# Kernel tuning notes

Measured on AMD Instinct MI355X. Metric: run time of the kernel, lower is better.

## Reference

```python
import jax, jax.numpy as jnp
import numpy as np

B, T, H, W = 8, 16, 512, 512
N, C = 300000, 128
STRIDE_B, STRIDE_T, STRIDE_H = T * H * W, H * W, W
SENTINEL = B * STRIDE_B  # out-of-range linear index used as unique fill_value


def setup_inputs() -> dict:
    key = jax.random.key(0)
    ks = jax.random.split(key, 8)
    # Random valid voxel coordinates via decomposed random linear index
    lin = jax.random.randint(ks[0], (N,), 0, SENTINEL, dtype=jnp.int32)
    b = lin // STRIDE_B
    r = lin % STRIDE_B
    t = r // STRIDE_T
    r = r % STRIDE_T
    y = r // STRIDE_H
    x = r % STRIDE_H
    indices = jnp.stack([b, t, y, x], axis=1).astype(jnp.int32)  # [N,4]
    s = 0.02
    return {
        "feats": jax.random.normal(ks[1], (N, C), jnp.float32),
        "indices": indices,
        "W1": jax.random.normal(ks[2], (C, C), jnp.float32) * s,
        "ln1_g": jnp.ones((C,), jnp.float32),
        "ln1_b": jnp.zeros((C,), jnp.float32),
        "W2": jax.random.normal(ks[3], (C, C), jnp.float32) * s,
        "ln2_g": jnp.ones((C,), jnp.float32),
        "ln2_b": jnp.zeros((C,), jnp.float32),
        "se_w1": jax.random.normal(ks[4], (C, C // 4), jnp.float32) * s,
        "se_b1": jnp.zeros((C // 4,), jnp.float32),
        "se_w2": jax.random.normal(ks[5], (C // 4, C), jnp.float32) * s,
        "se_b2": jnp.zeros((C,), jnp.float32),
    }


def _layernorm(x, g, b, eps=1e-5):
    mu = jnp.mean(x, axis=-1, keepdims=True)
    var = jnp.mean((x - mu) ** 2, axis=-1, keepdims=True)
    return (x - mu) * jax.lax.rsqrt(var + eps) * g + b


def reference(feats, indices, W1, ln1_g, ln1_b, W2, ln2_g, ln2_b,
              se_w1, se_b1, se_w2, se_b2):
    # conv1 (SubMConv3d k=1 == per-voxel linear) -> LayerNorm -> ReLU
    out = jax.nn.relu(_layernorm(feats @ W1, ln1_g, ln1_b))
    # conv2 -> LayerNorm
    out = _layernorm(out @ W2, ln2_g, ln2_b)
    # SE: global mean over all voxels -> fc -> relu -> fc -> sigmoid -> scale
    squeezed = jnp.mean(out, axis=0)                       # [C]
    scale = jax.nn.sigmoid(jax.nn.relu(squeezed @ se_w1 + se_b1) @ se_w2 + se_b2)
    out = out * scale
    # sparse_add(out, identity): linear hash, unique, scatter_add
    idx = indices.astype(jnp.int32)
    lin = (idx[:, 0] * STRIDE_B + idx[:, 1] * STRIDE_T
           + idx[:, 2] * STRIDE_H + idx[:, 3])             # [N]
    all_lin = jnp.concatenate([lin, lin])                  # [2N]
    all_feats = jnp.concatenate([out, feats])              # [2N, C]
    M = all_lin.shape[0]
    uniq, inv = jnp.unique(all_lin, size=M, fill_value=SENTINEL,
                           return_inverse=True)
    inv = inv.ravel()
    merged = jax.ops.segment_sum(all_feats, inv, num_segments=M)  # [2N, C]
    # decompose unique linear indices back to (b, t, y, x)
    cb = uniq // STRIDE_B
    r = uniq % STRIDE_B
    ct = r // STRIDE_T
    r = r % STRIDE_T
    ch = r // STRIDE_H
    cw = r % STRIDE_H
    comb_idx = jnp.stack([cb, ct, ch, cw], axis=1).astype(jnp.int32)
    # drop zero-feature / padded voxels (fixed-shape mask instead of compaction)
    valid = (jnp.abs(merged).sum(axis=1) > 1e-8) & (uniq < SENTINEL)
    merged = jnp.where(valid[:, None], merged, 0.0)
    merged = jax.nn.relu(merged)                           # lif2
    return merged, comb_idx, valid
```

## Files before the change

### kernel.cpp

```cpp
#include <hip/hip_runtime.h>
#include <cstdint>
#include <cstddef>

#define NVOX 300000
#define SB 4194304
#define ST 262144
#define SHH 512
#define SENT 33554432
#define NWORDS (SENT/64)

typedef __attribute__((ext_vector_type(8))) short short8;
typedef __attribute__((ext_vector_type(4))) float f32x4;

static __device__ __forceinline__ float bf2f(unsigned short u){
  return __uint_as_float(((unsigned)u) << 16);
}
static __device__ __forceinline__ unsigned short f2bf(float f){
  unsigned u = __float_as_uint(f);
  u = u + 0x7fffu + ((u >> 16) & 1u);
  return (unsigned short)(u >> 16);
}
static __device__ __forceinline__ short8 pack8(float4 a, float4 b){
  short8 s;
  s[0]=(short)f2bf(a.x); s[1]=(short)f2bf(a.y); s[2]=(short)f2bf(a.z); s[3]=(short)f2bf(a.w);
  s[4]=(short)f2bf(b.x); s[5]=(short)f2bf(b.y); s[6]=(short)f2bf(b.z); s[7]=(short)f2bf(b.w);
  return s;
}

static __device__ __forceinline__ unsigned rank_of(int l,
    const unsigned long long* __restrict__ bits,
    const unsigned* __restrict__ coarse,
    const unsigned* __restrict__ blockExcl){
  int w = l >> 6;
  unsigned long long m = 1ull << (l & 63);
  return coarse[w] + blockExcl[w >> 12]
       + (unsigned)__popcll(bits[w] & (m - 1ull));
}

__global__ void pack_w(const float* __restrict__ W, unsigned short* __restrict__ Wt){
  int i = blockIdx.x*256 + threadIdx.x;
  int j = i & 7, lane = (i >> 3) & 63, ks = (i >> 9) & 3, nt = i >> 11;
  int k = ks*32 + (lane >> 4)*8 + j;
  int n = nt*16 + (lane & 15);
  Wt[i] = f2bf(W[k*128 + n]);
}

__global__ void mark_kernel(const int* __restrict__ idx,
                            unsigned long long* __restrict__ bits,
                            unsigned long long* __restrict__ dupbits,
                            int* __restrict__ lin,
                            int* __restrict__ duplist,
                            int* __restrict__ dupcount){
  int i = blockIdx.x*256 + threadIdx.x;
  if(i >= NVOX) return;
  int4 v = ((const int4*)idx)[i];
  int l = v.x*SB + v.y*ST + v.z*SHH + v.w;
  lin[i] = l;
  unsigned long long m = 1ull << (l & 63);
  unsigned long long old = atomicOr(&bits[l >> 6], m);
  if(old & m){
    atomicOr(&dupbits[l >> 6], m);
    int s = atomicAdd(dupcount, 1);
    duplist[s] = i;
  }
}

__global__ void scan1_kernel(const unsigned long long* __restrict__ bits,
                             unsigned* __restrict__ coarse,
                             unsigned* __restrict__ blockSums){
  __shared__ unsigned sh[256];
  int t = threadIdx.x, blk = blockIdx.x;
  int w0 = blk*4096 + t*16;
  unsigned p[16]; unsigned s = 0;
  #pragma unroll
  for(int k=0;k<16;k++){ unsigned c = (unsigned)__popcll(bits[w0+k]); p[k] = s; s += c; }
  sh[t] = s; __syncthreads();
  for(int off=1; off<256; off<<=1){
    unsigned v = (t >= off) ? sh[t-off] : 0u;
    __syncthreads();
    sh[t] += v;
    __syncthreads();
  }
  unsigned texcl = (t == 0) ? 0u : sh[t-1];
  #pragma unroll
  for(int k=0;k<16;k++) coarse[w0+k] = texcl + p[k];
  if(t == 255) blockSums[blk] = sh[255];
}

__global__ void scan2_kernel(const unsigned* __restrict__ blockSums,
                             unsigned* __restrict__ blockExcl){
  __shared__ unsigned sh[128];
  int t = threadIdx.x;
  sh[t] = blockSums[t]; __syncthreads();
  for(int off=1; off<128; off<<=1){
    unsigned v = (t >= off) ? sh[t-off] : 0u;
    __syncthreads();
    sh[t] += v;
    __syncthreads();
  }
  if(t == 0) blockExcl[0] = 0u;
  blockExcl[t+1] = sh[t];
}

__global__ void emit_kernel(const unsigned long long* __restrict__ bits,
                            const unsigned* __restrict__ coarse,
                            const unsigned* __restrict__ blockExcl,
                            float* __restrict__ out_comb){
  int w = blockIdx.x*256 + threadIdx.x;
  if(w >= NWORDS) return;
  unsigned long long bw = bits[w];
  if(!bw) return;
  unsigned j = coarse[w] + blockExcl[w >> 12];
  while(bw){
    int p = __builtin_ctzll(bw);
    bw &= bw - 1;
    int v = (w << 6) | p;
    int cb = v >> 22;
    int r  = v & (SB - 1);
    int ct = r >> 18;
    r &= (ST - 1);
    int ch = r >> 9;
    int cw = r & 511;
    ((float4*)out_comb)[j] = make_float4((float)cb,(float)ct,(float)ch,(float)cw);
    j++;
  }
}

__global__ void zerodup_kernel(const int* __restrict__ duplist,
    const int* __restrict__ dupcount, const int* __restrict__ lin,
    const unsigned long long* __restrict__ bits,
    const unsigned* __restrict__ coarse, const unsigned* __restrict__ blockExcl,
    float* __restrict__ out_merged)
{
  int cnt = *dupcount;
  int lane = threadIdx.x & 63;
  for(int e = blockIdx.x*4 + (threadIdx.x >> 6); e < cnt; e += gridDim.x*4){
    int l = lin[duplist[e]];
    unsigned j = rank_of(l, bits, coarse, blockExcl);
    *(float2*)(out_merged + (size_t)j*128 + 2*lane) = make_float2(0.f, 0.f);
  }
}

__global__ __launch_bounds__(256) void fused_mlp(
    const float* __restrict__ X,
    const unsigned short* __restrict__ w1t, const float* __restrict__ g1v,
    const float* __restrict__ b1v,
    const unsigned short* __restrict__ w2t, const float* __restrict__ g2v,
    const float* __restrict__ b2v,
    unsigned short* __restrict__ Y, float* __restrict__ sq, int nrows)
{
  __shared__ __align__(16) unsigned short xs[64][136];
  __shared__ float sqs[4][128];
  const int t = threadIdx.x;
  const int rowbase = blockIdx.x * 64;
  const int wave = t >> 6, quad = (t >> 4) & 3, l15 = t & 15;
  const int wbase = wave * 16;
  const int lane8 = (t & 63) * 8;
  const int lrow = wbase + l15;
  const int grow = rowbase + lrow;
  const int kofs = quad * 8;
  const bool rv_a = grow < nrows;

  short8 a0, a1, a2, a3;
  {
    const float* xp = X + (size_t)grow * 128 + kofs;
    float4 z = make_float4(0.f,0.f,0.f,0.f);
    float4 u0=z,u1=z,u2=z,u3=z,u4=z,u5=z,u6=z,u7=z;
    if (rv_a) {
      u0 = ((const float4*)(xp      ))[0];
      u1 = ((const float4*)(xp +   4))[0];
      u2 = ((const float4*)(xp +  32))[0];
      u3 = ((const float4*)(xp +  36))[0];
      u4 = ((const float4*)(xp +  64))[0];
      u5 = ((const float4*)(xp +  68))[0];
      u6 = ((const float4*)(xp +  96))[0];
      u7 = ((const float4*)(xp + 100))[0];
    }
    a0 = pack8(u0, u1); a1 = pack8(u2, u3);
    a2 = pack8(u4, u5); a3 = pack8(u6, u7);
  }

  {
    f32x4 acc[8];
    #pragma unroll
    for (int nt = 0; nt < 8; nt++) {
      const unsigned short* wp = w1t + nt*2048 + lane8;
      short8 bv0 = *(const short8*)(wp);
      short8 bv1 = *(const short8*)(wp + 512);
      short8 bv2 = *(const short8*)(wp + 1024);
      short8 bv3 = *(const short8*)(wp + 1536);
      f32x4 c = {0.f,0.f,0.f,0.f};
      c = __builtin_amdgcn_mfma_f32_16x16x32_bf16(a0, bv0, c, 0, 0, 0);
      c = __builtin_amdgcn_mfma_f32_16x16x32_bf16(a1, bv1, c, 0, 0, 0);
      c = __builtin_amdgcn_mfma_f32_16x16x32_bf16(a2, bv2, c, 0, 0, 0);
      c = __builtin_amdgcn_mfma_f32_16x16x32_bf16(a3, bv3, c, 0, 0, 0);
      acc[nt] = c;
    }

    float gg[8], bb[8];
    #pragma unroll
    for (int nt = 0; nt < 8; nt++) {
      gg[nt] = g1v[nt*16 + l15]; bb[nt] = b1v[nt*16 + l15];
    }
    #pragma unroll
    for (int r = 0; r < 4; r++) {
      float s = 0.f, q = 0.f;
      #pragma unroll
      for (int nt = 0; nt < 8; nt++) { float v = acc[nt][r]; s += v; q += v*v; }
      #pragma unroll
      for (int mm = 1; mm < 16; mm <<= 1) { s += __shfl_xor(s, mm); q += __shfl_xor(q, mm); }
      float mu = s * (1.f/128.f);
      float var = fmaxf(q * (1.f/128.f) - mu*mu, 0.f);
      float rinv = rsqrtf(var + 1e-5f);
      int orow = wbase + quad*4 + r;
      #pragma unroll
      for (int nt = 0; nt < 8; nt++) {
        float v = (acc[nt][r] - mu) * rinv * gg[nt] + bb[nt];
        v = fmaxf(v, 0.f);
        xs[orow][nt*16 + l15] = f2bf(v);
      }
    }
  }

  {
    short8 c0 = *(const short8*)&xs[lrow][  0 + kofs];
    short8 c1 = *(const short8*)&xs[lrow][ 32 + kofs];
    short8 c2 = *(const short8*)&xs[lrow][ 64 + kofs];
    short8 c3 = *(const short8*)&xs[lrow][ 96 + kofs];

    f32x4 acc[8];
    #pragma unroll
    for (int nt = 0; nt < 8; nt++) {
      const unsigned short* wp = w2t + nt*2048 + lane8;
      short8 bv0 = *(const short8*)(wp);
      short8 bv1 = *(const short8*)(wp + 512);
      short8 bv2 = *(const short8*)(wp + 1024);
      short8 bv3 = *(const short8*)(wp + 1536);
      f32x4 c = {0.f,0.f,0.f,0.f};
      c = __builtin_amdgcn_mfma_f32_16x16x32_bf16(c0, bv0, c, 0, 0, 0);
      c = __builtin_amdgcn_mfma_f32_16x16x32_bf16(c1, bv1, c, 0, 0, 0);
      c = __builtin_amdgcn_mfma_f32_16x16x32_bf16(c2, bv2, c, 0, 0, 0);
      c = __builtin_amdgcn_mfma_f32_16x16x32_bf16(c3, bv3, c, 0, 0, 0);
      acc[nt] = c;
    }

    float gg[8], bb[8], ch[8];
    #pragma unroll
    for (int nt = 0; nt < 8; nt++) {
      gg[nt] = g2v[nt*16 + l15]; bb[nt] = b2v[nt*16 + l15]; ch[nt] = 0.f;
    }
    #pragma unroll
    for (int r = 0; r < 4; r++) {
      float s = 0.f, q = 0.f;
      #pragma unroll
      for (int nt = 0; nt < 8; nt++) { float v = acc[nt][r]; s += v; q += v*v; }
      #pragma unroll
      for (int mm = 1; mm < 16; mm <<= 1) { s += __shfl_xor(s, mm); q += __shfl_xor(q, mm); }
      float mu = s * (1.f/128.f);
      float var = fmaxf(q * (1.f/128.f) - mu*mu, 0.f);
      float rinv = rsqrtf(var + 1e-5f);
      int orow = wbase + quad*4 + r;
      bool rv = (rowbase + orow) < nrows;
      #pragma unroll
      for (int nt = 0; nt < 8; nt++) {
        float v = (acc[nt][r] - mu) * rinv * gg[nt] + bb[nt];
        if (rv) ch[nt] += v;
        xs[orow][nt*16 + l15] = f2bf(v);
      }
    }
    #pragma unroll
    for (int nt = 0; nt < 8; nt++) {
      float v = ch[nt];
      v += __shfl_xor(v, 16); v += __shfl_xor(v, 32);
      if (quad == 0) sqs[wave][nt*16 + l15] = v;
    }
  }

  __syncthreads();
  #pragma unroll
  for (int mm = 0; mm < 4; mm++) {
    int c = mm*256 + t;
    int row = c >> 4, s8 = c & 15;
    if (rowbase + row < nrows) {
      short8 v = *(const short8*)&xs[row][s8*8];
      *(short8*)(Y + (size_t)(rowbase+row)*128 + s8*8) = v;
    }
  }
  if (t < 128) atomicAdd(&sq[t], sqs[0][t] + sqs[1][t] + sqs[2][t] + sqs[3][t]);
}

__global__ void se_kernel(const float* __restrict__ sq, const float* __restrict__ w1,
    const float* __restrict__ b1, const float* __restrict__ w2,
    const float* __restrict__ b2, float* __restrict__ scale)
{
  __shared__ float mean[128];
  __shared__ float h1[32];
  int t = threadIdx.x;
  mean[t] = sq[t] * (1.f/(float)NVOX);
  __syncthreads();
  if(t < 32){
    float s = b1[t];
    for(int c=0;c<128;c++) s += mean[c]*w1[c*32+t];
    h1[t] = fmaxf(s, 0.f);
  }
  __syncthreads();
  float s = b2[t];
  for(int j=0;j<32;j++) s += h1[j]*w2[j*128+t];
  scale[t] = 1.f/(1.f + expf(-s));
}

__global__ void scatter_kernel(const unsigned short* __restrict__ y2,
    const float* __restrict__ feats, const float* __restrict__ scale,
    const int* __restrict__ lin, const unsigned long long* __restrict__ bits,
    const unsigned long long* __restrict__ dupbits,
    const unsigned* __restrict__ coarse, const unsigned* __restrict__ blockExcl,
    float* __restrict__ out_merged, float* __restrict__ out_valid)
{
  int row = blockIdx.x*4 + (threadIdx.x >> 6);
  int lane = threadIdx.x & 63;
  int l = lin[row];
  int w = l >> 6;
  unsigned long long m = 1ull << (l & 63);
  unsigned j = coarse[w] + blockExcl[w >> 12]
             + (unsigned)__popcll(bits[w] & (m - 1ull));
  size_t rb = (size_t)row * 128;
  unsigned yy = *(const unsigned*)(y2 + rb + 2*lane);
  float2 ff = *(const float2*)(feats + rb + 2*lane);
  float2 ss = *(const float2*)(scale + 2*lane);
  float v0 = bf2f((unsigned short)(yy & 0xffffu)) * ss.x + ff.x;
  float v1 = bf2f((unsigned short)(yy >> 16))     * ss.y + ff.y;
  size_t ob = (size_t)j * 128;
  if (dupbits[w] & m) {
    atomicAdd(out_merged + ob + 2*lane,     v0);
    atomicAdd(out_merged + ob + 2*lane + 1, v1);
  } else {
    float s = fabsf(v0) + fabsf(v1);
    #pragma unroll
    for(int mm=1; mm<64; mm<<=1) s += __shfl_xor(s, mm);
    bool valid = s > 1e-8f;
    float2 o;
    o.x = valid ? fmaxf(v0, 0.f) : 0.f;
    o.y = valid ? fmaxf(v1, 0.f) : 0.f;
    *(float2*)(out_merged + ob + 2*lane) = o;
    if (lane == 0) out_valid[j] = valid ? 1.f : 0.f;
  }
}

__global__ void dupfinal_kernel(const int* __restrict__ duplist,
    const int* __restrict__ dupcount, const int* __restrict__ lin,
    unsigned long long* __restrict__ dupbits,
    const unsigned long long* __restrict__ bits,
    const unsigned* __restrict__ coarse, const unsigned* __restrict__ blockExcl,
    float* __restrict__ out_merged, float* __restrict__ out_valid)
{
  int cnt = *dupcount;
  int lane = threadIdx.x & 63;
  for(int e = blockIdx.x*4 + (threadIdx.x >> 6); e < cnt; e += gridDim.x*4){
    int l = lin[duplist[e]];
    int w = l >> 6;
    unsigned long long m = 1ull << (l & 63);
    int claimed = 0;
    if (lane == 0){
      unsigned long long old = atomicAnd(&dupbits[w], ~m);
      claimed = (old & m) ? 1 : 0;
    }
    claimed = __shfl(claimed, 0);
    if (!claimed) continue;
    unsigned j = coarse[w] + blockExcl[w >> 12]
               + (unsigned)__popcll(bits[w] & (m - 1ull));
    size_t ob = (size_t)j * 128;
    float2 v = *(float2*)(out_merged + ob + 2*lane);
    float s = fabsf(v.x) + fabsf(v.y);
    #pragma unroll
    for(int mm=1; mm<64; mm<<=1) s += __shfl_xor(s, mm);
    bool valid = s > 1e-8f;
    float2 o;
    o.x = valid ? fmaxf(v.x, 0.f) : 0.f;
    o.y = valid ? fmaxf(v.y, 0.f) : 0.f;
    *(float2*)(out_merged + ob + 2*lane) = o;
    if (lane == 0) out_valid[j] = valid ? 1.f : 0.f;
  }
}

__global__ void padfill_kernel(const unsigned* __restrict__ blockExcl,
    float* __restrict__ out_merged, float* __restrict__ out_comb,
    float* __restrict__ out_valid)
{
  int lane = threadIdx.x & 63;
  int wv = threadIdx.x >> 6;
  if (blockIdx.x < 512) {
    unsigned U = blockExcl[128];
    for (unsigned r = U + blockIdx.x*4 + wv; r < NVOX; r += 512*4) {
      *(float2*)(out_merged + (size_t)r*128 + 2*lane) = make_float2(0.f, 0.f);
      if (lane == 0) {
        out_valid[r] = 0.f;
        ((float4*)out_comb)[r] = make_float4(8.f, 0.f, 0.f, 0.f);
      }
    }
  } else {
    int r = NVOX + (blockIdx.x - 512)*4 + wv;
    *(float2*)(out_merged + (size_t)r*128 + 2*lane) = make_float2(0.f, 0.f);
    if (lane == 0) {
      out_valid[r] = 0.f;
      ((float4*)out_comb)[r] = make_float4(8.f, 0.f, 0.f, 0.f);
    }
  }
}

extern "C" void kernel_launch(void* const* d_in, const int* in_sizes, int n_in,
                              void* d_out, int out_size, void* d_ws, size_t ws_size,
                              hipStream_t stream)
{
  const float* feats   = (const float*)d_in[0];
  const int*   indices = (const int*)d_in[1];
  const float* W1  = (const float*)d_in[2];
  const float* g1  = (const float*)d_in[3];
  const float* b1  = (const float*)d_in[4];
  const float* W2  = (const float*)d_in[5];
  const float* g2  = (const float*)d_in[6];
  const float* b2  = (const float*)d_in[7];
  const float* sw1 = (const float*)d_in[8];
  const float* sb1 = (const float*)d_in[9];
  const float* sw2 = (const float*)d_in[10];
  const float* sb2 = (const float*)d_in[11];

  float* out_merged = (float*)d_out;
  float* out_comb   = out_merged + (size_t)2*NVOX*128;
  float* out_valid  = out_comb   + (size_t)2*NVOX*4;

  char* cur = (char*)d_ws;
  auto alloc = [&](size_t b) -> void* {
    void* p = (void*)cur;
    cur += (b + 255) & ~(size_t)255;
    return p;
  };
  unsigned short*      y2        = (unsigned short*)alloc((size_t)NVOX*128*2);
  unsigned long long*  bits      = (unsigned long long*)alloc((size_t)NWORDS*8);
  unsigned long long*  dupbits   = (unsigned long long*)alloc((size_t)NWORDS*8);
  unsigned*            coarse    = (unsigned*)alloc((size_t)NWORDS*4);
  unsigned*            blockSums = (unsigned*)alloc(128*4);
  unsigned*            blockExcl = (unsigned*)alloc(129*4);
  float*               sq        = (float*)alloc(128*4);
  int*                 dupcount  = (int*)alloc(4);
  float*               scale     = (float*)alloc(128*4);
  int*                 lin       = (int*)alloc((size_t)NVOX*4);
  int*                 duplist   = (int*)alloc((size_t)NVOX*4);
  unsigned short*      w1t       = (unsigned short*)alloc(128*128*2);
  unsigned short*      w2t       = (unsigned short*)alloc(128*128*2);

  hipMemsetAsync(bits, 0, (size_t)NWORDS*8*2, stream);
  hipMemsetAsync(sq, 0, 512 + 256, stream);

  pack_w<<<64, 256, 0, stream>>>(W1, w1t);
  pack_w<<<64, 256, 0, stream>>>(W2, w2t);

  mark_kernel<<<(NVOX+255)/256, 256, 0, stream>>>(indices, bits, dupbits, lin,
                                                  duplist, dupcount);
  scan1_kernel<<<128, 256, 0, stream>>>(bits, coarse, blockSums);
  scan2_kernel<<<1, 128, 0, stream>>>(blockSums, blockExcl);
  emit_kernel<<<NWORDS/256, 256, 0, stream>>>(bits, coarse, blockExcl, out_comb);
  zerodup_kernel<<<512, 256, 0, stream>>>(duplist, dupcount, lin, bits, coarse,
                                          blockExcl, out_merged);

  fused_mlp<<<(NVOX+63)/64, 256, 0, stream>>>(feats, w1t, g1, b1, w2t, g2, b2,
                                              y2, sq, NVOX);
  se_kernel<<<1, 128, 0, stream>>>(sq, sw1, sb1, sw2, sb2, scale);

  scatter_kernel<<<NVOX/4, 256, 0, stream>>>(y2, feats, scale, lin, bits, dupbits,
                                             coarse, blockExcl, out_merged, out_valid);
  dupfinal_kernel<<<512, 256, 0, stream>>>(duplist, dupcount, lin, dupbits, bits,
                                           coarse, blockExcl, out_merged, out_valid);
  padfill_kernel<<<512 + NVOX/4, 256, 0, stream>>>(blockExcl, out_merged,
                                                   out_comb, out_valid);
}
```

Measured before the change: 667.5 us.

## Stage MLP weights in LDS and process two row tiles per wave

The fused MLP kernel now copies each 128x128 bf16 weight matrix into shared memory once per block and has each wave compute two 16-row tiles, so every B-fragment load feeds two MFMAs. The goal is less global/L2 weight traffic per row and fewer blocks. The price is about 67KB of LDS per block, which lowers occupancy, plus extra syncthreads. The output write-back changes to a per-wave layout. The fused MLP is only one of several kernels in the pipeline.

```diff
diff --git a/kernel.cpp b/kernel.cpp
--- a/kernel.cpp
+++ b/kernel.cpp
@@ -141,6 +141,7 @@
   }
 }
 
+#define MLP_ROWS 128
 __global__ __launch_bounds__(256) void fused_mlp(
     const float* __restrict__ X,
     const unsigned short* __restrict__ w1t, const float* __restrict__ g1v,
@@ -149,24 +150,30 @@
     const float* __restrict__ b2v,
     unsigned short* __restrict__ Y, float* __restrict__ sq, int nrows)
 {
-  __shared__ __align__(16) unsigned short xs[64][136];
+  __shared__ __align__(16) unsigned short wlds[16384];
+  __shared__ __align__(16) unsigned short xs[128][136];
   __shared__ float sqs[4][128];
   const int t = threadIdx.x;
-  const int rowbase = blockIdx.x * 64;
+  const int rowbase = blockIdx.x * MLP_ROWS;
   const int wave = t >> 6, quad = (t >> 4) & 3, l15 = t & 15;
-  const int wbase = wave * 16;
+  const int wbase = wave * 32;
   const int lane8 = (t & 63) * 8;
-  const int lrow = wbase + l15;
-  const int grow = rowbase + lrow;
   const int kofs = quad * 8;
-  const bool rv_a = grow < nrows;
-
-  short8 a0, a1, a2, a3;
+  const int grow0 = rowbase + wbase + l15;
+  const int grow1 = grow0 + 16;
+  const bool rv0 = grow0 < nrows, rv1 = grow1 < nrows;
+
+  #pragma unroll
+  for (int m = 0; m < 8; m++)
+    ((float4*)wlds)[m*256 + t] = ((const float4*)w1t)[m*256 + t];
+
+  short8 a0,a1,a2,a3,a4,a5,a6,a7;
   {
-    const float* xp = X + (size_t)grow * 128 + kofs;
     float4 z = make_float4(0.f,0.f,0.f,0.f);
     float4 u0=z,u1=z,u2=z,u3=z,u4=z,u5=z,u6=z,u7=z;
-    if (rv_a) {
+    float4 w0=z,w1=z,w2=z,w3=z,w4=z,w5=z,w6=z,w7=z;
+    if (rv0) {
+      const float* xp = X + (size_t)grow0 * 128 + kofs;
       u0 = ((const float4*)(xp      ))[0];
       u1 = ((const float4*)(xp +   4))[0];
       u2 = ((const float4*)(xp +  32))[0];
@@ -176,25 +183,43 @@
       u6 = ((const float4*)(xp +  96))[0];
       u7 = ((const float4*)(xp + 100))[0];
     }
+    if (rv1) {
+      const float* xp = X + (size_t)grow1 * 128 + kofs;
+      w0 = ((const float4*)(xp      ))[0];
+      w1 = ((const float4*)(xp +   4))[0];
+      w2 = ((const float4*)(xp +  32))[0];
+      w3 = ((const float4*)(xp +  36))[0];
+      w4 = ((const float4*)(xp +  64))[0];
+      w5 = ((const float4*)(xp +  68))[0];
+      w6 = ((const float4*)(xp +  96))[0];
+      w7 = ((const float4*)(xp + 100))[0];
+    }
     a0 = pack8(u0, u1); a1 = pack8(u2, u3);
     a2 = pack8(u4, u5); a3 = pack8(u6, u7);
-  }
+    a4 = pack8(w0, w1); a5 = pack8(w2, w3);
+    a6 = pack8(w4, w5); a7 = pack8(w6, w7);
+  }
+  __syncthreads();
 
   {
-    f32x4 acc[8];
+    f32x4 acc0[8], acc1[8];
     #pragma unroll
     for (int nt = 0; nt < 8; nt++) {
-      const unsigned short* wp = w1t + nt*2048 + lane8;
+      const unsigned short* wp = wlds + nt*2048 + lane8;
       short8 bv0 = *(const short8*)(wp);
       short8 bv1 = *(const short8*)(wp + 512);
       short8 bv2 = *(const short8*)(wp + 1024);
       short8 bv3 = *(const short8*)(wp + 1536);
-      f32x4 c = {0.f,0.f,0.f,0.f};
-      c = __builtin_amdgcn_mfma_f32_16x16x32_bf16(a0, bv0, c, 0, 0, 0);
-      c = __builtin_amdgcn_mfma_f32_16x16x32_bf16(a1, bv1, c, 0, 0, 0);
-      c = __builtin_amdgcn_mfma_f32_16x16x32_bf16(a2, bv2, c, 0, 0, 0);
-      c = __builtin_amdgcn_mfma_f32_16x16x32_bf16(a3, bv3, c, 0, 0, 0);
-      acc[nt] = c;
+      f32x4 c0 = {0.f,0.f,0.f,0.f}, c1 = {0.f,0.f,0.f,0.f};
+      c0 = __builtin_amdgcn_mfma_f32_16x16x32_bf16(a0, bv0, c0, 0, 0, 0);
+      c1 = __builtin_amdgcn_mfma_f32_16x16x32_bf16(a4, bv0, c1, 0, 0, 0);
+      c0 = __builtin_amdgcn_mfma_f32_16x16x32_bf16(a1, bv1, c0, 0, 0, 0);
+      c1 = __builtin_amdgcn_mfma_f32_16x16x32_bf16(a5, bv1, c1, 0, 0, 0);
+      c0 = __builtin_amdgcn_mfma_f32_16x16x32_bf16(a2, bv2, c0, 0, 0, 0);
+      c1 = __builtin_amdgcn_mfma_f32_16x16x32_bf16(a6, bv2, c1, 0, 0, 0);
+      c0 = __builtin_amdgcn_mfma_f32_16x16x32_bf16(a3, bv3, c0, 0, 0, 0);
+      c1 = __builtin_amdgcn_mfma_f32_16x16x32_bf16(a7, bv3, c1, 0, 0, 0);
+      acc0[nt] = c0; acc1[nt] = c1;
     }
 
     float gg[8], bb[8];
@@ -203,45 +228,64 @@
       gg[nt] = g1v[nt*16 + l15]; bb[nt] = b1v[nt*16 + l15];
     }
     #pragma unroll
-    for (int r = 0; r < 4; r++) {
-      float s = 0.f, q = 0.f;
+    for (int tile = 0; tile < 2; tile++) {
       #pragma unroll
-      for (int nt = 0; nt < 8; nt++) { float v = acc[nt][r]; s += v; q += v*v; }
-      #pragma unroll
-      for (int mm = 1; mm < 16; mm <<= 1) { s += __shfl_xor(s, mm); q += __shfl_xor(q, mm); }
-      float mu = s * (1.f/128.f);
-      float var = fmaxf(q * (1.f/128.f) - mu*mu, 0.f);
-      float rinv = rsqrtf(var + 1e-5f);
-      int orow = wbase + quad*4 + r;
-      #pragma unroll
-      for (int nt = 0; nt < 8; nt++) {
-        float v = (acc[nt][r] - mu) * rinv * gg[nt] + bb[nt];
-        v = fmaxf(v, 0.f);
-        xs[orow][nt*16 + l15] = f2bf(v);
+      for (int r = 0; r < 4; r++) {
+        float s = 0.f, q = 0.f;
+        #pragma unroll
+        for (int nt = 0; nt < 8; nt++) {
+          float v = tile ? acc1[nt][r] : acc0[nt][r]; s += v; q += v*v;
+        }
+        #pragma unroll
+        for (int mm = 1; mm < 16; mm <<= 1) { s += __shfl_xor(s, mm); q += __shfl_xor(q, mm); }
+        float mu = s * (1.f/128.f);
+        float var = fmaxf(q * (1.f/128.f) - mu*mu, 0.f);
+        float rinv = rsqrtf(var + 1e-5f);
+        int orow = wbase + tile*16 + quad*4 + r;
+        #pragma unroll
+        for (int nt = 0; nt < 8; nt++) {
+          float v = ((tile ? acc1[nt][r] : acc0[nt][r]) - mu) * rinv * gg[nt] + bb[nt];
+          v = fmaxf(v, 0.f);
+          xs[orow][nt*16 + l15] = f2bf(v);
+        }
       }
     }
   }
+  __syncthreads();
+
+  #pragma unroll
+  for (int m = 0; m < 8; m++)
+    ((float4*)wlds)[m*256 + t] = ((const float4*)w2t)[m*256 + t];
+
+  short8 p0 = *(const short8*)&xs[wbase + l15][  0 + kofs];
+  short8 p1 = *(const short8*)&xs[wbase + l15][ 32 + kofs];
+  short8 p2 = *(const short8*)&xs[wbase + l15][ 64 + kofs];
+  short8 p3 = *(const short8*)&xs[wbase + l15][ 96 + kofs];
+  short8 p4 = *(const short8*)&xs[wbase + 16 + l15][  0 + kofs];
+  short8 p5 = *(const short8*)&xs[wbase + 16 + l15][ 32 + kofs];
+  short8 p6 = *(const short8*)&xs[wbase + 16 + l15][ 64 + kofs];
+  short8 p7 = *(const short8*)&xs[wbase + 16 + l15][ 96 + kofs];
+  __syncthreads();
 
   {
-    short8 c0 = *(const short8*)&xs[lrow][  0 + kofs];
-    short8 c1 = *(const short8*)&xs[lrow][ 32 + kofs];
-    short8 c2 = *(const short8*)&xs[lrow][ 64 + kofs];
-    short8 c3 = *(const short8*)&xs[lrow][ 96 + kofs];
-
-    f32x4 acc[8];
+    f32x4 acc0[8], acc1[8];
     #pragma unroll
     for (int nt = 0; nt < 8; nt++) {
-      const unsigned short* wp = w2t + nt*2048 + lane8;
+      const unsigned short* wp = wlds + nt*2048 + lane8;
       short8 bv0 = *(const short8*)(wp);
       short8 bv1 = *(const short8*)(wp + 512);
       short8 bv2 = *(const short8*)(wp + 1024);
       short8 bv3 = *(const short8*)(wp + 1536);
-      f32x4 c = {0.f,0.f,0.f,0.f};
-      c = __builtin_amdgcn_mfma_f32_16x16x32_bf16(c0, bv0, c, 0, 0, 0);
-      c = __builtin_amdgcn_mfma_f32_16x16x32_bf16(c1, bv1, c, 0, 0, 0);
-      c = __builtin_amdgcn_mfma_f32_16x16x32_bf16(c2, bv2, c, 0, 0, 0);
-      c = __builtin_amdgcn_mfma_f32_16x16x32_bf16(c3, bv3, c, 0, 0, 0);
-      acc[nt] = c;
+      f32x4 c0 = {0.f,0.f,0.f,0.f}, c1 = {0.f,0.f,0.f,0.f};
+      c0 = __builtin_amdgcn_mfma_f32_16x16x32_bf16(p0, bv0, c0, 0, 0, 0);
+      c1 = __builtin_amdgcn_mfma_f32_16x16x32_bf16(p4, bv0, c1, 0, 0, 0);
+      c0 = __builtin_amdgcn_mfma_f32_16x16x32_bf16(p1, bv1, c0, 0, 0, 0);
+      c1 = __builtin_amdgcn_mfma_f32_16x16x32_bf16(p5, bv1, c1, 0, 0, 0);
+      c0 = __builtin_amdgcn_mfma_f32_16x16x32_bf16(p2, bv2, c0, 0, 0, 0);
+      c1 = __builtin_amdgcn_mfma_f32_16x16x32_bf16(p6, bv2, c1, 0, 0, 0);
+      c0 = __builtin_amdgcn_mfma_f32_16x16x32_bf16(p3, bv3, c0, 0, 0, 0);
+      c1 = __builtin_amdgcn_mfma_f32_16x16x32_bf16(p7, bv3, c1, 0, 0, 0);
+      acc0[nt] = c0; acc1[nt] = c1;
     }
 
     float gg[8], bb[8], ch[8];
@@ -250,22 +294,27 @@
       gg[nt] = g2v[nt*16 + l15]; bb[nt] = b2v[nt*16 + l15]; ch[nt] = 0.f;
     }
     #pragma unroll
-    for (int r = 0; r < 4; r++) {
-      float s = 0.f, q = 0.f;
+    for (int tile = 0; tile < 2; tile++) {
       #pragma unroll
-      for (int nt = 0; nt < 8; nt++) { float v = acc[nt][r]; s += v; q += v*v; }
-      #pragma unroll
-      for (int mm = 1; mm < 16; mm <<= 1) { s += __shfl_xor(s, mm); q += __shfl_xor(q, mm); }
-      float mu = s * (1.f/128.f);
-      float var = fmaxf(q * (1.f/128.f) - mu*mu, 0.f);
-      float rinv = rsqrtf(var + 1e-5f);
-      int orow = wbase + quad*4 + r;
-      bool rv = (rowbase + orow) < nrows;
-      #pragma unroll
-      for (int nt = 0; nt < 8; nt++) {
-        float v = (acc[nt][r] - mu) * rinv * gg[nt] + bb[nt];
-        if (rv) ch[nt] += v;
-        xs[orow][nt*16 + l15] = f2bf(v);
+      for (int r = 0; r < 4; r++) {
+        float s = 0.f, q = 0.f;
+        #pragma unroll
+        for (int nt = 0; nt < 8; nt++) {
+          float v = tile ? acc1[nt][r] : acc0[nt][r]; s += v; q += v*v;
+        }
+        #pragma unroll
+        for (int mm = 1; mm < 16; mm <<= 1) { s += __shfl_xor(s, mm); q += __shfl_xor(q, mm); }
+        float mu = s * (1.f/128.f);
+        float var = fmaxf(q * (1.f/128.f) - mu*mu, 0.f);
+        float rinv = rsqrtf(var + 1e-5f);
+        int orow = wbase + tile*16 + quad*4 + r;
+        bool rv = (rowbase + orow) < nrows;
+        #pragma unroll
+        for (int nt = 0; nt < 8; nt++) {
+          float v = ((tile ? acc1[nt][r] : acc0[nt][r]) - mu) * rinv * gg[nt] + bb[nt];
+          if (rv) ch[nt] += v;
+          xs[orow][nt*16 + l15] = f2bf(v);
+        }
       }
     }
     #pragma unroll
@@ -276,16 +325,16 @@
     }
   }
 
+  #pragma unroll
+  for (int mm = 0; mm < 8; mm++) {
+    int c = mm*64 + (t & 63);
+    int rl = wbase + (c >> 4), s8 = c & 15;
+    if (rowbase + rl < nrows) {
+      short8 v = *(const short8*)&xs[rl][s8*8];
+      *(short8*)(Y + (size_t)(rowbase+rl)*128 + s8*8) = v;
+    }
+  }
   __syncthreads();
-  #pragma unroll
-  for (int mm = 0; mm < 4; mm++) {
-    int c = mm*256 + t;
-    int row = c >> 4, s8 = c & 15;
-    if (rowbase + row < nrows) {
-      short8 v = *(const short8*)&xs[row][s8*8];
-      *(short8*)(Y + (size_t)(rowbase+row)*128 + s8*8) = v;
-    }
-  }
   if (t < 128) atomicAdd(&sq[t], sqs[0][t] + sqs[1][t] + sqs[2][t] + sqs[3][t]);
 }
 
@@ -462,8 +511,8 @@
   zerodup_kernel<<<512, 256, 0, stream>>>(duplist, dupcount, lin, bits, coarse,
                                           blockExcl, out_merged);
 
-  fused_mlp<<<(NVOX+63)/64, 256, 0, stream>>>(feats, w1t, g1, b1, w2t, g2, b2,
-                                              y2, sq, NVOX);
+  fused_mlp<<<(NVOX + MLP_ROWS - 1)/MLP_ROWS, 256, 0, stream>>>(
+      feats, w1t, g1, b1, w2t, g2, b2, y2, sq, NVOX);
   se_kernel<<<1, 128, 0, stream>>>(sq, sw1, sb1, sw2, sb2, scale);
 
   scatter_kernel<<<NVOX/4, 256, 0, stream>>>(y2, feats, scale, lin, bits, dupbits,
```

Result: faster. 619.6 us (-7.2%).
